# Kernel tuning notes

Measured on AMD Instinct MI355X. Metric: run time of the kernel, lower is better.

## Reference

```python
import jax, jax.numpy as jnp
import numpy as np

D_MODEL = 1024
OUTPUT_DIM = 1024
NUM_HEADS = 16
HEAD_DIM = D_MODEL // NUM_HEADS


def _xavier(key, shape):
    fan_in, fan_out = shape[1], shape[0]
    limit = float(np.sqrt(6.0 / (fan_in + fan_out)))
    return jax.random.uniform(key, shape, jnp.float32, -limit, limit)


def setup_inputs() -> dict:
    key = jax.random.key(0)
    k_h, k_q, k_k, k_o = jax.random.split(key, 4)
    H = jax.random.normal(k_h, (2, 2048, D_MODEL), dtype=jnp.float32)
    # nn.Linear weights are [out, in]; xavier_uniform on weights, default (uniform) biases left as zeros-equivalent
    Wq = _xavier(k_q, (D_MODEL, D_MODEL))
    bq = jnp.zeros((D_MODEL,), jnp.float32)
    Wk = _xavier(k_k, (D_MODEL, D_MODEL))
    bk = jnp.zeros((D_MODEL,), jnp.float32)
    Wo = _xavier(k_o, (OUTPUT_DIM, D_MODEL))
    bo = jnp.zeros((OUTPUT_DIM,), jnp.float32)
    return {"H": H, "Wq": Wq, "bq": bq, "Wk": Wk, "bk": bk, "Wo": Wo, "bo": bo}


def reference(H, Wq, bq, Wk, bk, Wo, bo):
    B, S, _ = H.shape
    Q = H @ Wq.T + bq  # [B,S,D]
    K = H @ Wk.T + bk
    # split heads -> [B,nh,S,hd]
    Qh = Q.reshape(B, S, NUM_HEADS, HEAD_DIM).transpose(0, 2, 1, 3)
    Kh = K.reshape(B, S, NUM_HEADS, HEAD_DIM).transpose(0, 2, 1, 3)
    Vh = H.reshape(B, S, NUM_HEADS, HEAD_DIM).transpose(0, 2, 1, 3)
    scale = 1.0 / jnp.sqrt(jnp.float32(HEAD_DIM))
    A = jnp.einsum('bhqd,bhkd->bhqk', Qh, Kh) * scale  # [B,nh,S,S]
    A = jax.nn.softmax(A, axis=-1)
    out = jnp.einsum('bhqk,bhkd->bhqd', A, Vh)  # [B,nh,S,hd]
    out = out.transpose(0, 2, 1, 3).reshape(B, S, D_MODEL)
    return out @ Wo.T + bo
```

## Files before the change

### kernel.cpp

```cpp
#include <hip/hip_runtime.h>
#include <stdint.h>

#define BB 2
#define SS 2048
#define DD 1024
#define NH 16
#define HD 64
#define MM 4096

typedef __bf16 bf16x8 __attribute__((ext_vector_type(8)));
typedef float  f32x4  __attribute__((ext_vector_type(4)));

__device__ __forceinline__ unsigned short f2bf(float f) {
    __bf16 h = (__bf16)f;
    return __builtin_bit_cast(unsigned short, h);
}

__device__ __forceinline__ void async_cp16(const void* g, const void* l) {
    __builtin_amdgcn_global_load_lds(
        (const __attribute__((address_space(1))) void*)(uintptr_t)g,
        (__attribute__((address_space(3))) void*)(uint32_t)(uintptr_t)l,
        16, 0, 0);
}

__device__ __forceinline__ f32x4 mfma16(bf16x8 a, bf16x8 b, f32x4 c) {
    return __builtin_amdgcn_mfma_f32_16x16x32_bf16(a, b, c, 0, 0, 0);
}

__global__ __launch_bounds__(256) void k_cvtw(const float* __restrict__ Wq,
                                              const float* __restrict__ Wk,
                                              const float* __restrict__ Wo,
                                              unsigned short* __restrict__ Wqb,
                                              unsigned short* __restrict__ Wkb,
                                              unsigned short* __restrict__ Wob) {
    int g = blockIdx.x;
    const float* src; unsigned short* dst; int base;
    if (g < 512)       { src = Wq; dst = Wqb; base = g; }
    else if (g < 1024) { src = Wk; dst = Wkb; base = g - 512; }
    else               { src = Wo; dst = Wob; base = g - 1024; }
    int i = (base * 256 + threadIdx.x) * 8;
    float4 a = *(const float4*)(src + i);
    float4 b = *(const float4*)(src + i + 4);
    unsigned short o[8];
    o[0] = f2bf(a.x); o[1] = f2bf(a.y); o[2] = f2bf(a.z); o[3] = f2bf(a.w);
    o[4] = f2bf(b.x); o[5] = f2bf(b.y); o[6] = f2bf(b.z); o[7] = f2bf(b.w);
    *(ulonglong2*)(dst + i) = *(ulonglong2*)o;
}

__global__ __launch_bounds__(256) void k_prep(const float* __restrict__ H,
                                              unsigned short* __restrict__ Hb,
                                              unsigned short* __restrict__ Vt) {
    __shared__ float tile[128][68];
    const int sb = blockIdx.x, h = blockIdx.y, b = blockIdx.z;
    const int t = threadIdx.x;
    const int col4 = t & 15;
    const int srow0 = t >> 4;
#pragma unroll
    for (int p = 0; p < 8; ++p) {
        int s = p * 16 + srow0;
        float4 v = *(const float4*)(H + (size_t)(b * SS + sb * 128 + s) * DD + h * HD + col4 * 4);
        *(float4*)&tile[s][col4 * 4] = v;
    }
    __syncthreads();
#pragma unroll
    for (int it = 0; it < 4; ++it) {
        int task = it * 256 + t;
        int s = task >> 3;
        int dg = task & 7;
        unsigned short pk[8];
#pragma unroll
        for (int j = 0; j < 8; ++j) pk[j] = f2bf(tile[s][dg * 8 + j]);
        *(ulonglong2*)(Hb + (size_t)(b * SS + sb * 128 + s) * DD + h * HD + dg * 8) = *(ulonglong2*)pk;
    }
#pragma unroll
    for (int it = 0; it < 4; ++it) {
        int task = it * 256 + t;
        int d = task >> 4;
        int sg = task & 15;
        unsigned short pk[8];
#pragma unroll
        for (int j = 0; j < 8; ++j) pk[j] = f2bf(tile[sg * 8 + j][d]);
        *(ulonglong2*)(Vt + (size_t)((b * NH + h) * HD + d) * SS + sb * 128 + sg * 8) = *(ulonglong2*)pk;
    }
}

template <bool BF16OUT>
__device__ __forceinline__ void gemm_body(const unsigned short* __restrict__ A,
                                          const unsigned short* __restrict__ Bt,
                                          const float* __restrict__ bias,
                                          void* __restrict__ Cp, float oscale) {
    __shared__ unsigned short lsA[128 * 32];
    __shared__ unsigned short lsB[128 * 32];
    const int tid = threadIdx.x;
    const int lane = tid & 63;
    const int w = tid >> 6;
    const int wm = w & 1, wn = w >> 1;
    const int r = lane & 15, quad = lane >> 4;
    const int mBase = blockIdx.y * 128;
    const int nBase = blockIdx.x * 128;

    f32x4 acc[4][4];
#pragma unroll
    for (int i = 0; i < 4; ++i)
#pragma unroll
        for (int j = 0; j < 4; ++j) acc[i][j] = f32x4{0.f, 0.f, 0.f, 0.f};

    for (int kb = 0; kb < 32; ++kb) {
        __syncthreads();
#pragma unroll
        for (int t = 0; t < 2; ++t) {
            int l = t * 256 + tid;
            int c = l ^ ((l >> 3) & 7);
            int row = c >> 2, kc = c & 3;
            async_cp16(A + (size_t)(mBase + row) * 1024 + kb * 32 + kc * 8, lsA + l * 8);
            async_cp16(Bt + (size_t)(nBase + row) * 1024 + kb * 32 + kc * 8, lsB + l * 8);
        }
        __syncthreads();

        bf16x8 af[4], bf[4];
#pragma unroll
        for (int mt = 0; mt < 4; ++mt) {
            int rowA = wm * 64 + mt * 16 + r;
            int c = rowA * 4 + quad;
            int l = c ^ ((c >> 3) & 7);
            af[mt] = *(const bf16x8*)(lsA + l * 8);
        }
#pragma unroll
        for (int nt = 0; nt < 4; ++nt) {
            int rowB = wn * 64 + nt * 16 + r;
            int c = rowB * 4 + quad;
            int l = c ^ ((c >> 3) & 7);
            bf[nt] = *(const bf16x8*)(lsB + l * 8);
        }
#pragma unroll
        for (int mt = 0; mt < 4; ++mt)
#pragma unroll
            for (int nt = 0; nt < 4; ++nt)
                acc[mt][nt] = mfma16(af[mt], bf[nt], acc[mt][nt]);
    }

    float bv[4];
#pragma unroll
    for (int nt = 0; nt < 4; ++nt) bv[nt] = bias[nBase + wn * 64 + nt * 16 + r];
#pragma unroll
    for (int mt = 0; mt < 4; ++mt)
#pragma unroll
        for (int nt = 0; nt < 4; ++nt) {
            int colg = nBase + wn * 64 + nt * 16 + r;
#pragma unroll
            for (int reg = 0; reg < 4; ++reg) {
                int rowg = mBase + wm * 64 + mt * 16 + quad * 4 + reg;
                float v = (acc[mt][nt][reg] + bv[nt]) * oscale;
                if (BF16OUT)
                    ((unsigned short*)Cp)[(size_t)rowg * 1024 + colg] = f2bf(v);
                else
                    ((float*)Cp)[(size_t)rowg * 1024 + colg] = v;
            }
        }
}

#define QSCALE 0.1803368801111137f

__global__ __launch_bounds__(256) void k_gemm_qk(const unsigned short* __restrict__ Hb,
                                                 const unsigned short* __restrict__ Wqb,
                                                 const unsigned short* __restrict__ Wkb,
                                                 const float* __restrict__ bq,
                                                 const float* __restrict__ bk,
                                                 unsigned short* __restrict__ Q,
                                                 unsigned short* __restrict__ K) {
    const unsigned short* Bt = blockIdx.z ? Wkb : Wqb;
    const float* bias = blockIdx.z ? bk : bq;
    unsigned short* C = blockIdx.z ? K : Q;
    float os = blockIdx.z ? 1.0f : QSCALE;
    gemm_body<true>(Hb, Bt, bias, C, os);
}

__global__ __launch_bounds__(256) void k_gemm_out(const unsigned short* __restrict__ Ctx,
                                                  const unsigned short* __restrict__ Wob,
                                                  const float* __restrict__ bo,
                                                  float* __restrict__ Out) {
    gemm_body<false>(Ctx, Wob, bo, Out, 1.0f);
}

__global__ __launch_bounds__(256) void k_attn(const unsigned short* __restrict__ Q,
                                              const unsigned short* __restrict__ K,
                                              const unsigned short* __restrict__ Vt,
                                              unsigned short* __restrict__ Ctx) {
    __shared__ unsigned short lsK[2][64 * 64];
    __shared__ unsigned short lsV[2][64 * 64];
    __shared__ unsigned short lsP[4 * 16 * 64];
    const int tid = threadIdx.x;
    const int lane = tid & 63;
    const int w = tid >> 6;
    const int r = lane & 15, quad = lane >> 4;
    const int qb = blockIdx.x, h = blockIdx.y, b = blockIdx.z;

    const int qrow = qb * 64 + w * 16 + r;
    const size_t qoff = (size_t)(b * SS + qrow) * DD + h * HD;
    bf16x8 aq[2];
    aq[0] = *(const bf16x8*)(Q + qoff + quad * 8);
    aq[1] = *(const bf16x8*)(Q + qoff + 32 + quad * 8);

    f32x4 accO[4];
#pragma unroll
    for (int nt = 0; nt < 4; ++nt) accO[nt] = f32x4{0.f, 0.f, 0.f, 0.f};
    float lsum[4] = {0.f, 0.f, 0.f, 0.f};

    unsigned short* Pw = lsP + w * 1024;

    auto stage = [&](int buf, int kt) {
#pragma unroll
        for (int t = 0; t < 2; ++t) {
            int l = t * 256 + tid;
            int c = l ^ ((l >> 3) & 7);
            int row = c >> 3, kc = c & 7;
            async_cp16(K + (size_t)(b * SS + kt * 64 + row) * DD + h * HD + kc * 8, lsK[buf] + l * 8);
            async_cp16(Vt + (size_t)((b * NH + h) * HD + row) * SS + kt * 64 + kc * 8, lsV[buf] + l * 8);
        }
    };

    stage(0, 0);
    for (int kt = 0; kt < 32; ++kt) {
        const int cur = kt & 1;
        __syncthreads();
        if (kt + 1 < 32) stage(cur ^ 1, kt + 1);

        f32x4 s[4];
#pragma unroll
        for (int nt = 0; nt < 4; ++nt) s[nt] = f32x4{0.f, 0.f, 0.f, 0.f};
#pragma unroll
        for (int t = 0; t < 2; ++t)
#pragma unroll
            for (int nt = 0; nt < 4; ++nt) {
                int rowK = nt * 16 + r;
                int c = rowK * 8 + t * 4 + quad;
                int l = c ^ ((c >> 3) & 7);
                bf16x8 bk = *(const bf16x8*)(lsK[cur] + l * 8);
                s[nt] = mfma16(aq[t], bk, s[nt]);
            }

#pragma unroll
        for (int reg = 0; reg < 4; ++reg) {
            float p0 = __builtin_amdgcn_exp2f(s[0][reg]);
            float p1 = __builtin_amdgcn_exp2f(s[1][reg]);
            float p2 = __builtin_amdgcn_exp2f(s[2][reg]);
            float p3 = __builtin_amdgcn_exp2f(s[3][reg]);
            lsum[reg] += (p0 + p1) + (p2 + p3);
            int prow = quad * 4 + reg;
            unsigned short* Pr = Pw + prow * 64;
            int ch0 = (0 + (r >> 3)) ^ (prow & 7);
            int ch1 = (2 + (r >> 3)) ^ (prow & 7);
            int ch2 = (4 + (r >> 3)) ^ (prow & 7);
            int ch3 = (6 + (r >> 3)) ^ (prow & 7);
            int sub = r & 7;
            Pr[ch0 * 8 + sub] = f2bf(p0);
            Pr[ch1 * 8 + sub] = f2bf(p1);
            Pr[ch2 * 8 + sub] = f2bf(p2);
            Pr[ch3 * 8 + sub] = f2bf(p3);
        }

#pragma unroll
        for (int t = 0; t < 2; ++t) {
            int cP = r * 8 + t * 4 + quad;
            int lP = cP ^ ((cP >> 3) & 7);
            bf16x8 ap = *(const bf16x8*)(Pw + lP * 8);
#pragma unroll
            for (int nt = 0; nt < 4; ++nt) {
                int rowV = nt * 16 + r;
                int cV = rowV * 8 + t * 4 + quad;
                int lV = cV ^ ((cV >> 3) & 7);
                bf16x8 bv = *(const bf16x8*)(lsV[cur] + lV * 8);
                accO[nt] = mfma16(ap, bv, accO[nt]);
            }
        }
    }

    float linv[4];
#pragma unroll
    for (int reg = 0; reg < 4; ++reg) {
        float l = lsum[reg];
        l += __shfl_xor(l, 1);
        l += __shfl_xor(l, 2);
        l += __shfl_xor(l, 4);
        l += __shfl_xor(l, 8);
        linv[reg] = 1.0f / l;
    }
#pragma unroll
    for (int nt = 0; nt < 4; ++nt) {
        int d = nt * 16 + r;
#pragma unroll
        for (int reg = 0; reg < 4; ++reg) {
            int qr = qb * 64 + w * 16 + quad * 4 + reg;
            Ctx[(size_t)(b * SS + qr) * DD + h * HD + d] = f2bf(accO[nt][reg] * linv[reg]);
        }
    }
}

extern "C" void kernel_launch(void* const* d_in, const int* in_sizes, int n_in,
                              void* d_out, int out_size, void* d_ws, size_t ws_size,
                              hipStream_t stream) {
    (void)in_sizes; (void)n_in; (void)out_size; (void)ws_size;
    const float* H  = (const float*)d_in[0];
    const float* Wq = (const float*)d_in[1];
    const float* bq = (const float*)d_in[2];
    const float* Wk = (const float*)d_in[3];
    const float* bk = (const float*)d_in[4];
    const float* Wo = (const float*)d_in[5];
    const float* bo = (const float*)d_in[6];
    float* Out = (float*)d_out;

    char* ws = (char*)d_ws;
    unsigned short* Hb  = (unsigned short*)(ws);
    unsigned short* Qb  = (unsigned short*)(ws + 8388608);
    unsigned short* Kb  = (unsigned short*)(ws + 16777216);
    unsigned short* Ctx = (unsigned short*)(ws + 25165824);
    unsigned short* Vt  = (unsigned short*)(ws + 33554432);
    unsigned short* Wqb = (unsigned short*)(ws + 41943040);
    unsigned short* Wkb = (unsigned short*)(ws + 44040192);
    unsigned short* Wob = (unsigned short*)(ws + 46137344);

    k_cvtw<<<dim3(1536), dim3(256), 0, stream>>>(Wq, Wk, Wo, Wqb, Wkb, Wob);
    k_prep<<<dim3(16, NH, BB), dim3(256), 0, stream>>>(H, Hb, Vt);
    k_gemm_qk<<<dim3(8, 32, 2), dim3(256), 0, stream>>>(Hb, Wqb, Wkb, bq, bk, Qb, Kb);
    k_attn<<<dim3(32, NH, BB), dim3(256), 0, stream>>>(Qb, Kb, Vt, Ctx);
    k_gemm_out<<<dim3(8, 32, 1), dim3(256), 0, stream>>>(Ctx, Wob, bo, Out);
}
```

Before: 202.4 us.

## Double-buffer GEMM loads, shrink M tile, and vectorize attention P stores

The GEMM body now double-buffers its LDS tiles, issuing async loads for the next K-slice before computing the current one. This removes one barrier per iteration and overlaps memory with MFMA. The M tile shrinks to 64, doubling the grid for better CU coverage at the cost of less reuse per block. In attention, global/LDS offsets are precomputed, and K rows are permuted within each tile so each lane can write its four P values as one 8-byte store instead of four scalar stores. The permutation relies on P and V staying consistent in key order.

```diff
diff --git a/kernel.cpp b/kernel.cpp
--- a/kernel.cpp
+++ b/kernel.cpp
@@ -9,6 +9,7 @@
 #define MM 4096
 
 typedef __bf16 bf16x8 __attribute__((ext_vector_type(8)));
+typedef __bf16 bf16x4 __attribute__((ext_vector_type(4)));
 typedef float  f32x4  __attribute__((ext_vector_type(4)));
 
 __device__ __forceinline__ unsigned short f2bf(float f) {
@@ -84,56 +85,81 @@
     }
 }
 
-template <bool BF16OUT>
+template <int TM, bool BF16OUT>
 __device__ __forceinline__ void gemm_body(const unsigned short* __restrict__ A,
                                           const unsigned short* __restrict__ Bt,
                                           const float* __restrict__ bias,
                                           void* __restrict__ Cp, float oscale) {
-    __shared__ unsigned short lsA[128 * 32];
-    __shared__ unsigned short lsB[128 * 32];
+    constexpr int MT = TM / 32;
+    constexpr int AR = (TM * 4) / 256;
+    __shared__ unsigned short lsA[2][TM * 32];
+    __shared__ unsigned short lsB[2][128 * 32];
     const int tid = threadIdx.x;
     const int lane = tid & 63;
     const int w = tid >> 6;
     const int wm = w & 1, wn = w >> 1;
     const int r = lane & 15, quad = lane >> 4;
-    const int mBase = blockIdx.y * 128;
+    const int mBase = blockIdx.y * TM;
     const int nBase = blockIdx.x * 128;
 
-    f32x4 acc[4][4];
-#pragma unroll
-    for (int i = 0; i < 4; ++i)
+    const unsigned short* gA[AR]; uint laOff[AR];
+#pragma unroll
+    for (int t = 0; t < AR; ++t) {
+        int l = t * 256 + tid;
+        int c = l ^ ((l >> 3) & 7);
+        int row = c >> 2, kc = c & 3;
+        gA[t] = A + (size_t)(mBase + row) * 1024 + kc * 8;
+        laOff[t] = l * 8;
+    }
+    const unsigned short* gB[2]; uint lbOff[2];
+#pragma unroll
+    for (int t = 0; t < 2; ++t) {
+        int l = t * 256 + tid;
+        int c = l ^ ((l >> 3) & 7);
+        int row = c >> 2, kc = c & 3;
+        gB[t] = Bt + (size_t)(nBase + row) * 1024 + kc * 8;
+        lbOff[t] = l * 8;
+    }
+    uint aOff[MT], bOff[4];
+#pragma unroll
+    for (int mt = 0; mt < MT; ++mt) {
+        int rowA = wm * (TM / 2) + mt * 16 + r;
+        int c = rowA * 4 + quad;
+        aOff[mt] = (uint)((c ^ ((c >> 3) & 7)) * 8);
+    }
+#pragma unroll
+    for (int nt = 0; nt < 4; ++nt) {
+        int rowB = wn * 64 + nt * 16 + r;
+        int c = rowB * 4 + quad;
+        bOff[nt] = (uint)((c ^ ((c >> 3) & 7)) * 8);
+    }
+
+    f32x4 acc[MT][4];
+#pragma unroll
+    for (int i = 0; i < MT; ++i)
 #pragma unroll
         for (int j = 0; j < 4; ++j) acc[i][j] = f32x4{0.f, 0.f, 0.f, 0.f};
 
+    auto stage = [&](int buf) {
+#pragma unroll
+        for (int t = 0; t < AR; ++t) { async_cp16(gA[t], &lsA[buf][laOff[t]]); gA[t] += 32; }
+#pragma unroll
+        for (int t = 0; t < 2; ++t)  { async_cp16(gB[t], &lsB[buf][lbOff[t]]); gB[t] += 32; }
+    };
+
+    stage(0);
     for (int kb = 0; kb < 32; ++kb) {
+        const int cur = kb & 1;
         __syncthreads();
-#pragma unroll
-        for (int t = 0; t < 2; ++t) {
-            int l = t * 256 + tid;
-            int c = l ^ ((l >> 3) & 7);
-            int row = c >> 2, kc = c & 3;
-            async_cp16(A + (size_t)(mBase + row) * 1024 + kb * 32 + kc * 8, lsA + l * 8);
-            async_cp16(Bt + (size_t)(nBase + row) * 1024 + kb * 32 + kc * 8, lsB + l * 8);
-        }
-        __syncthreads();
-
-        bf16x8 af[4], bf[4];
-#pragma unroll
-        for (int mt = 0; mt < 4; ++mt) {
-            int rowA = wm * 64 + mt * 16 + r;
-            int c = rowA * 4 + quad;
-            int l = c ^ ((c >> 3) & 7);
-            af[mt] = *(const bf16x8*)(lsA + l * 8);
-        }
-#pragma unroll
-        for (int nt = 0; nt < 4; ++nt) {
-            int rowB = wn * 64 + nt * 16 + r;
-            int c = rowB * 4 + quad;
-            int l = c ^ ((c >> 3) & 7);
-            bf[nt] = *(const bf16x8*)(lsB + l * 8);
-        }
-#pragma unroll
-        for (int mt = 0; mt < 4; ++mt)
+        if (kb + 1 < 32) stage(cur ^ 1);
+
+        bf16x8 af[MT], bf[4];
+#pragma unroll
+        for (int mt = 0; mt < MT; ++mt) af[mt] = *(const bf16x8*)&lsA[cur][aOff[mt]];
+#pragma unroll
+        for (int nt = 0; nt < 4; ++nt)  bf[nt] = *(const bf16x8*)&lsB[cur][bOff[nt]];
+#pragma unroll
+        for (int mt = 0; mt < MT; ++mt)
 #pragma unroll
             for (int nt = 0; nt < 4; ++nt)
                 acc[mt][nt] = mfma16(af[mt], bf[nt], acc[mt][nt]);
@@ -143,13 +169,13 @@
 #pragma unroll
     for (int nt = 0; nt < 4; ++nt) bv[nt] = bias[nBase + wn * 64 + nt * 16 + r];
 #pragma unroll
-    for (int mt = 0; mt < 4; ++mt)
+    for (int mt = 0; mt < MT; ++mt)
 #pragma unroll
         for (int nt = 0; nt < 4; ++nt) {
             int colg = nBase + wn * 64 + nt * 16 + r;
 #pragma unroll
             for (int reg = 0; reg < 4; ++reg) {
-                int rowg = mBase + wm * 64 + mt * 16 + quad * 4 + reg;
+                int rowg = mBase + wm * (TM / 2) + mt * 16 + quad * 4 + reg;
                 float v = (acc[mt][nt][reg] + bv[nt]) * oscale;
                 if (BF16OUT)
                     ((unsigned short*)Cp)[(size_t)rowg * 1024 + colg] = f2bf(v);
@@ -172,14 +198,14 @@
     const float* bias = blockIdx.z ? bk : bq;
     unsigned short* C = blockIdx.z ? K : Q;
     float os = blockIdx.z ? 1.0f : QSCALE;
-    gemm_body<true>(Hb, Bt, bias, C, os);
+    gemm_body<64, true>(Hb, Bt, bias, C, os);
 }
 
 __global__ __launch_bounds__(256) void k_gemm_out(const unsigned short* __restrict__ Ctx,
                                                   const unsigned short* __restrict__ Wob,
                                                   const float* __restrict__ bo,
                                                   float* __restrict__ Out) {
-    gemm_body<false>(Ctx, Wob, bo, Out, 1.0f);
+    gemm_body<64, false>(Ctx, Wob, bo, Out, 1.0f);
 }
 
 __global__ __launch_bounds__(256) void k_attn(const unsigned short* __restrict__ Q,
@@ -206,24 +232,50 @@
     for (int nt = 0; nt < 4; ++nt) accO[nt] = f32x4{0.f, 0.f, 0.f, 0.f};
     float lsum[4] = {0.f, 0.f, 0.f, 0.f};
 
+    const unsigned short* gK[2]; const unsigned short* gV[2]; uint lO[2];
+#pragma unroll
+    for (int t = 0; t < 2; ++t) {
+        int l = t * 256 + tid;
+        int c = l ^ ((l >> 3) & 7);
+        int row = c >> 3, kc = c & 7;
+        int srow = 4 * (row & 15) + (row >> 4);
+        gK[t] = K + (size_t)(b * SS + srow) * DD + h * HD + kc * 8;
+        gV[t] = Vt + (size_t)((b * NH + h) * HD + row) * SS + kc * 8;
+        lO[t] = l * 8;
+    }
+    uint off[2][4];
+#pragma unroll
+    for (int t = 0; t < 2; ++t)
+#pragma unroll
+        for (int nt = 0; nt < 4; ++nt) {
+            int rowX = nt * 16 + r;
+            int c = rowX * 8 + t * 4 + quad;
+            off[t][nt] = (uint)((c ^ ((c >> 3) & 7)) * 8);
+        }
+    uint pw[4], pr[2];
+#pragma unroll
+    for (int reg = 0; reg < 4; ++reg) {
+        int prow = quad * 4 + reg;
+        pw[reg] = (uint)(prow * 64 + ((r >> 1) ^ (prow & 7)) * 8 + (r & 1) * 4);
+    }
+#pragma unroll
+    for (int t = 0; t < 2; ++t)
+        pr[t] = (uint)(r * 64 + ((4 * t + quad) ^ (r & 7)) * 8);
     unsigned short* Pw = lsP + w * 1024;
 
-    auto stage = [&](int buf, int kt) {
+    auto stage = [&](int buf) {
 #pragma unroll
         for (int t = 0; t < 2; ++t) {
-            int l = t * 256 + tid;
-            int c = l ^ ((l >> 3) & 7);
-            int row = c >> 3, kc = c & 7;
-            async_cp16(K + (size_t)(b * SS + kt * 64 + row) * DD + h * HD + kc * 8, lsK[buf] + l * 8);
-            async_cp16(Vt + (size_t)((b * NH + h) * HD + row) * SS + kt * 64 + kc * 8, lsV[buf] + l * 8);
+            async_cp16(gK[t], &lsK[buf][lO[t]]); gK[t] += 64 * DD;
+            async_cp16(gV[t], &lsV[buf][lO[t]]); gV[t] += 64;
         }
     };
 
-    stage(0, 0);
+    stage(0);
     for (int kt = 0; kt < 32; ++kt) {
         const int cur = kt & 1;
         __syncthreads();
-        if (kt + 1 < 32) stage(cur ^ 1, kt + 1);
+        if (kt + 1 < 32) stage(cur ^ 1);
 
         f32x4 s[4];
 #pragma unroll
@@ -231,13 +283,8 @@
 #pragma unroll
         for (int t = 0; t < 2; ++t)
 #pragma unroll
-            for (int nt = 0; nt < 4; ++nt) {
-                int rowK = nt * 16 + r;
-                int c = rowK * 8 + t * 4 + quad;
-                int l = c ^ ((c >> 3) & 7);
-                bf16x8 bk = *(const bf16x8*)(lsK[cur] + l * 8);
-                s[nt] = mfma16(aq[t], bk, s[nt]);
-            }
+            for (int nt = 0; nt < 4; ++nt)
+                s[nt] = mfma16(aq[t], *(const bf16x8*)&lsK[cur][off[t][nt]], s[nt]);
 
 #pragma unroll
         for (int reg = 0; reg < 4; ++reg) {
@@ -246,32 +293,16 @@
             float p2 = __builtin_amdgcn_exp2f(s[2][reg]);
             float p3 = __builtin_amdgcn_exp2f(s[3][reg]);
             lsum[reg] += (p0 + p1) + (p2 + p3);
-            int prow = quad * 4 + reg;
-            unsigned short* Pr = Pw + prow * 64;
-            int ch0 = (0 + (r >> 3)) ^ (prow & 7);
-            int ch1 = (2 + (r >> 3)) ^ (prow & 7);
-            int ch2 = (4 + (r >> 3)) ^ (prow & 7);
-            int ch3 = (6 + (r >> 3)) ^ (prow & 7);
-            int sub = r & 7;
-            Pr[ch0 * 8 + sub] = f2bf(p0);
-            Pr[ch1 * 8 + sub] = f2bf(p1);
-            Pr[ch2 * 8 + sub] = f2bf(p2);
-            Pr[ch3 * 8 + sub] = f2bf(p3);
+            bf16x4 pk = {(__bf16)p0, (__bf16)p1, (__bf16)p2, (__bf16)p3};
+            *(bf16x4*)&Pw[pw[reg]] = pk;
         }
 
 #pragma unroll
         for (int t = 0; t < 2; ++t) {
-            int cP = r * 8 + t * 4 + quad;
-            int lP = cP ^ ((cP >> 3) & 7);
-            bf16x8 ap = *(const bf16x8*)(Pw + lP * 8);
-#pragma unroll
-            for (int nt = 0; nt < 4; ++nt) {
-                int rowV = nt * 16 + r;
-                int cV = rowV * 8 + t * 4 + quad;
-                int lV = cV ^ ((cV >> 3) & 7);
-                bf16x8 bv = *(const bf16x8*)(lsV[cur] + lV * 8);
-                accO[nt] = mfma16(ap, bv, accO[nt]);
-            }
+            bf16x8 ap = *(const bf16x8*)&Pw[pr[t]];
+#pragma unroll
+            for (int nt = 0; nt < 4; ++nt)
+                accO[nt] = mfma16(ap, *(const bf16x8*)&lsV[cur][off[t][nt]], accO[nt]);
         }
     }
 
@@ -321,7 +352,7 @@
 
     k_cvtw<<<dim3(1536), dim3(256), 0, stream>>>(Wq, Wk, Wo, Wqb, Wkb, Wob);
     k_prep<<<dim3(16, NH, BB), dim3(256), 0, stream>>>(H, Hb, Vt);
-    k_gemm_qk<<<dim3(8, 32, 2), dim3(256), 0, stream>>>(Hb, Wqb, Wkb, bq, bk, Qb, Kb);
+    k_gemm_qk<<<dim3(8, 64, 2), dim3(256), 0, stream>>>(Hb, Wqb, Wkb, bq, bk, Qb, Kb);
     k_attn<<<dim3(32, NH, BB), dim3(256), 0, stream>>>(Qb, Kb, Vt, Ctx);
-    k_gemm_out<<<dim3(8, 32, 1), dim3(256), 0, stream>>>(Ctx, Wob, bo, Out);
-}
+    k_gemm_out<<<dim3(8, 64, 1), dim3(256), 0, stream>>>(Ctx, Wob, bo, Out);
+}
```

After: 201.8 us. Within noise of the previous version (-0.3%).
